# Optimization experiments

Hardware: AMD Instinct MI355X
Metric: run time of the kernel (lower is better)

Reference implementation:

```python
import jax, jax.numpy as jnp
import numpy as np

IDENT_SIZE = 100000
E = 1024      # embedding_dim == lstm input size
H = 2048      # hidden_dim
R = 1024      # remainder_dim
RULES = 50000 # rules_size


def setup_inputs() -> dict:
    key = jax.random.key(0)
    ks = jax.random.split(key, 12)
    def w(k, shape, scale=0.02):
        return jax.random.normal(k, shape, dtype=jnp.float32) * scale
    return {
        "ident": jax.random.randint(ks[0], (1,), 0, IDENT_SIZE),
        "remainder": jax.random.normal(ks[1], (1, 1, R), dtype=jnp.float32),
        "h0": jax.random.normal(ks[2], (1, 1, H), dtype=jnp.float32),
        "c0": jax.random.normal(ks[3], (1, 1, H), dtype=jnp.float32),
        "emb": w(ks[4], (IDENT_SIZE, E)),
        "W_rin": w(ks[5], (R, E)),   # linear_remainder_in, stored [in, out]
        "b_rin": jnp.zeros((E,), jnp.float32),
        "W_ih": w(ks[6], (4 * H, E)),  # torch LSTM weight_ih_l0, gate order i,f,g,o
        "W_hh": w(ks[7], (4 * H, H)),  # torch LSTM weight_hh_l0
        "b_ih": jnp.zeros((4 * H,), jnp.float32),
        "b_hh": jnp.zeros((4 * H,), jnp.float32),
        "W_ro": w(ks[8], (H, R)),      # linear_remainder_out
        "b_ro": jnp.zeros((R,), jnp.float32),
        "W_out": w(ks[9], (H, RULES)),  # linear_out
        "b_out": jnp.zeros((RULES,), jnp.float32),
    }


def reference(ident, remainder, h0, c0, emb, W_rin, b_rin, W_ih, W_hh,
              b_ih, b_hh, W_ro, b_ro, W_out, b_out):
    # embeds = embedding(ident).view((1,-1))  -> [1, E]
    embeds = emb[ident].reshape(1, -1)
    # inputs = embeds + relu(linear_remainder_in(remainder)) -> broadcast [1,1,E]
    x = embeds + jax.nn.relu(remainder @ W_rin + b_rin)  # [1,1,E]
    # single-step LSTM (seq=1, batch=1), torch gate order i, f, g, o
    gates = x @ W_ih.T + b_ih + h0 @ W_hh.T + b_hh  # [1,1,4H]
    i, f, g, o = jnp.split(gates, 4, axis=-1)
    c = jax.nn.sigmoid(f) * c0 + jax.nn.sigmoid(i) * jnp.tanh(g)
    h = jax.nn.sigmoid(o) * jnp.tanh(c)  # lstm_out == h for seq=1
    remainder_out = jax.nn.relu(h @ W_ro + b_ro)             # [1,1,R]
    out = jax.nn.log_softmax(jax.nn.relu(h @ W_out + b_out), axis=2)  # [1,1,RULES]
    return (out, (h, c), remainder_out)
```

## Files before the change

kernel.cpp:

```cpp
#include <hip/hip_runtime.h>
#include <math.h>

#define E_DIM 1024
#define H_DIM 2048
#define R_DIM 1024
#define RULES 50000

#define OUT_H  50000
#define OUT_C  52048
#define OUT_RO 54096

#define WS_XP    0
#define WS_X     8192
#define WS_H     9216
#define WS_PL    11264
#define WS_LOG   411264
#define WS_BSUM  461264
#define WS_PRO   461320

__device__ __forceinline__ float sigf(float x) { return 1.f / (1.f + expf(-x)); }

__global__ __launch_bounds__(256) void k_x_partial(const float* __restrict__ rem,
    const float* __restrict__ W_rin, float* __restrict__ xp)
{
    __shared__ float rs[128];
    int ec = blockIdx.x, rc = blockIdx.y;
    if (threadIdx.x < 128) rs[threadIdx.x] = rem[rc * 128 + threadIdx.x];
    __syncthreads();
    int e = ec * 256 + threadIdx.x;
    const float* base = W_rin + (size_t)rc * 128 * E_DIM + e;
    float acc = 0.f;
#pragma unroll 8
    for (int rr = 0; rr < 128; ++rr)
        acc = fmaf(rs[rr], base[(size_t)rr * E_DIM], acc);
    xp[rc * E_DIM + e] = acc;
}

__global__ __launch_bounds__(256) void k_x_final(const float* __restrict__ xp,
    const float* __restrict__ b_rin, const float* __restrict__ emb,
    const int* __restrict__ ident, float* __restrict__ x)
{
    int e = blockIdx.x * 256 + threadIdx.x;
    float s = 0.f;
#pragma unroll
    for (int rc = 0; rc < 8; ++rc) s += xp[rc * E_DIM + e];
    long long row = (long long)ident[0] * E_DIM;
    x[e] = emb[row + e] + fmaxf(s + b_rin[e], 0.f);
}

__global__ __launch_bounds__(256) void k_lstm(const float* __restrict__ x,
    const float* __restrict__ h0, const float* __restrict__ c0,
    const float* __restrict__ W_ih, const float* __restrict__ W_hh,
    const float* __restrict__ b_ih, const float* __restrict__ b_hh,
    float* __restrict__ d_out, float* __restrict__ ws_h)
{
    int k = blockIdx.x;
    int w = threadIdx.x >> 6, lane = threadIdx.x & 63;
    int j = w * H_DIM + k;
    const float4* Wi = (const float4*)(W_ih + (size_t)j * E_DIM);
    const float4* Wh = (const float4*)(W_hh + (size_t)j * H_DIM);
    const float4* x4 = (const float4*)x;
    const float4* h4 = (const float4*)h0;
    float acc = 0.f;
#pragma unroll
    for (int s = 0; s < 4; ++s) {
        int idx = s * 64 + lane;
        float4 wv = Wi[idx], xv = x4[idx];
        acc += wv.x * xv.x + wv.y * xv.y + wv.z * xv.z + wv.w * xv.w;
    }
#pragma unroll
    for (int s = 0; s < 8; ++s) {
        int idx = s * 64 + lane;
        float4 wv = Wh[idx], hv = h4[idx];
        acc += wv.x * hv.x + wv.y * hv.y + wv.z * hv.z + wv.w * hv.w;
    }
#pragma unroll
    for (int off = 32; off > 0; off >>= 1) acc += __shfl_xor(acc, off);
    __shared__ float gl[4];
    if (lane == 0) gl[w] = acc + b_ih[j] + b_hh[j];
    __syncthreads();
    if (threadIdx.x == 0) {
        float gi = gl[0], gf = gl[1], gg = gl[2], go = gl[3];
        float c = sigf(gf) * c0[k] + sigf(gi) * tanhf(gg);
        float h = sigf(go) * tanhf(c);
        d_out[OUT_H + k] = h;
        d_out[OUT_C + k] = c;
        ws_h[k] = h;
    }
}

__global__ __launch_bounds__(256) void k_logits_partial(const float* __restrict__ h,
    const float* __restrict__ W_out, float* __restrict__ pl)
{
    __shared__ float hs[256];
    int hc = blockIdx.y;
    hs[threadIdx.x] = h[hc * 256 + threadIdx.x];
    __syncthreads();
    int j0 = blockIdx.x * 1024 + threadIdx.x * 4;
    if (j0 >= RULES) return;
    float4 acc = {0.f, 0.f, 0.f, 0.f};
    const float* base = W_out + (size_t)hc * 256 * RULES + j0;
#pragma unroll 8
    for (int hh = 0; hh < 256; ++hh) {
        float hv = hs[hh];
        float4 wv = *(const float4*)(base + (size_t)hh * RULES);
        acc.x = fmaf(hv, wv.x, acc.x);
        acc.y = fmaf(hv, wv.y, acc.y);
        acc.z = fmaf(hv, wv.z, acc.z);
        acc.w = fmaf(hv, wv.w, acc.w);
    }
    *(float4*)(pl + (size_t)hc * RULES + j0) = acc;
}

__global__ __launch_bounds__(256) void k_ro_partial(const float* __restrict__ h,
    const float* __restrict__ W_ro, float* __restrict__ pro)
{
    __shared__ float hs[128];
    int hc = blockIdx.x;
    if (threadIdx.x < 128) hs[threadIdx.x] = h[hc * 128 + threadIdx.x];
    __syncthreads();
    int j0 = threadIdx.x * 4;
    float4 acc = {0.f, 0.f, 0.f, 0.f};
    const float* base = W_ro + (size_t)hc * 128 * R_DIM + j0;
#pragma unroll 8
    for (int hh = 0; hh < 128; ++hh) {
        float hv = hs[hh];
        float4 wv = *(const float4*)(base + (size_t)hh * R_DIM);
        acc.x = fmaf(hv, wv.x, acc.x);
        acc.y = fmaf(hv, wv.y, acc.y);
        acc.z = fmaf(hv, wv.z, acc.z);
        acc.w = fmaf(hv, wv.w, acc.w);
    }
    *(float4*)(pro + hc * R_DIM + j0) = acc;
}

__global__ __launch_bounds__(256) void k_logit_final(const float* __restrict__ pl,
    const float* __restrict__ b_out, float* __restrict__ logits,
    float* __restrict__ bsum)
{
    int j0 = blockIdx.x * 1024 + threadIdx.x * 4;
    float se = 0.f;
    if (j0 < RULES) {
        float4 s = {0.f, 0.f, 0.f, 0.f};
#pragma unroll
        for (int hc = 0; hc < 8; ++hc) {
            float4 p = *(const float4*)(pl + (size_t)hc * RULES + j0);
            s.x += p.x; s.y += p.y; s.z += p.z; s.w += p.w;
        }
        float4 b = *(const float4*)(b_out + j0);
        float4 l;
        l.x = fmaxf(s.x + b.x, 0.f);
        l.y = fmaxf(s.y + b.y, 0.f);
        l.z = fmaxf(s.z + b.z, 0.f);
        l.w = fmaxf(s.w + b.w, 0.f);
        *(float4*)(logits + j0) = l;
        se = expf(l.x) + expf(l.y) + expf(l.z) + expf(l.w);
    }
    __shared__ float red[256];
    red[threadIdx.x] = se;
    __syncthreads();
    for (int off = 128; off > 0; off >>= 1) {
        if (threadIdx.x < off) red[threadIdx.x] += red[threadIdx.x + off];
        __syncthreads();
    }
    if (threadIdx.x == 0) bsum[blockIdx.x] = red[0];
}

__global__ __launch_bounds__(256) void k_ro_final(const float* __restrict__ pro,
    const float* __restrict__ b_ro, float* __restrict__ out_ro)
{
    int j0 = threadIdx.x * 4;
    float4 s = {0.f, 0.f, 0.f, 0.f};
#pragma unroll
    for (int hc = 0; hc < 16; ++hc) {
        float4 p = *(const float4*)(pro + hc * R_DIM + j0);
        s.x += p.x; s.y += p.y; s.z += p.z; s.w += p.w;
    }
    float4 b = *(const float4*)(b_ro + j0);
    float4 o;
    o.x = fmaxf(s.x + b.x, 0.f);
    o.y = fmaxf(s.y + b.y, 0.f);
    o.z = fmaxf(s.z + b.z, 0.f);
    o.w = fmaxf(s.w + b.w, 0.f);
    *(float4*)(out_ro + j0) = o;
}

__global__ __launch_bounds__(256) void k_out(const float* __restrict__ logits,
    const float* __restrict__ bsum, float* __restrict__ d_out)
{
    __shared__ float lse_s;
    if (threadIdx.x == 0) {
        float s = 0.f;
        for (int i = 0; i < 49; ++i) s += bsum[i];
        lse_s = logf(s);
    }
    __syncthreads();
    int j = blockIdx.x * 256 + threadIdx.x;
    if (j < RULES) d_out[j] = logits[j] - lse_s;
}

extern "C" void kernel_launch(void* const* d_in, const int* in_sizes, int n_in,
                              void* d_out, int out_size, void* d_ws, size_t ws_size,
                              hipStream_t stream)
{
    const int*   ident = (const int*)  d_in[0];
    const float* rem   = (const float*)d_in[1];
    const float* h0    = (const float*)d_in[2];
    const float* c0    = (const float*)d_in[3];
    const float* emb   = (const float*)d_in[4];
    const float* W_rin = (const float*)d_in[5];
    const float* b_rin = (const float*)d_in[6];
    const float* W_ih  = (const float*)d_in[7];
    const float* W_hh  = (const float*)d_in[8];
    const float* b_ih  = (const float*)d_in[9];
    const float* b_hh  = (const float*)d_in[10];
    const float* W_ro  = (const float*)d_in[11];
    const float* b_ro  = (const float*)d_in[12];
    const float* W_out = (const float*)d_in[13];
    const float* b_out = (const float*)d_in[14];
    float* out = (float*)d_out;
    float* ws  = (float*)d_ws;

    k_x_partial<<<dim3(4, 8), 256, 0, stream>>>(rem, W_rin, ws + WS_XP);
    k_x_final<<<4, 256, 0, stream>>>(ws + WS_XP, b_rin, emb, ident, ws + WS_X);
    k_lstm<<<2048, 256, 0, stream>>>(ws + WS_X, h0, c0, W_ih, W_hh, b_ih, b_hh,
                                     out, ws + WS_H);
    k_logits_partial<<<dim3(49, 8), 256, 0, stream>>>(ws + WS_H, W_out, ws + WS_PL);
    k_ro_partial<<<16, 256, 0, stream>>>(ws + WS_H, W_ro, ws + WS_PRO);
    k_logit_final<<<49, 256, 0, stream>>>(ws + WS_PL, b_out, ws + WS_LOG, ws + WS_BSUM);
    k_ro_final<<<1, 256, 0, stream>>>(ws + WS_PRO, b_ro, out + OUT_RO);
    k_out<<<196, 256, 0, stream>>>(ws + WS_LOG, ws + WS_BSUM, out);
}
```

Before: 128.7 us.

## Fuse x-final into LSTM, merge logits/remainder kernels, split hidden dim 16-way

Folds the input-vector finalisation into each LSTM block, which rebuilds x in shared memory and so drops one launch. The logits and remainder-out partial GEMVs are merged into one launch, as are their reduce kernels. The logits split over the hidden dimension goes from 8 to 16 chunks, doubling block count for better bandwidth use. In exchange, every LSTM block redundantly reads the 8 x-partials and the embedding row, and the partial-sum buffer and its reduction double in size.

```diff
diff --git a/kernel.cpp b/kernel.cpp
--- a/kernel.cpp
+++ b/kernel.cpp
@@ -11,12 +11,11 @@
 #define OUT_RO 54096
 
 #define WS_XP    0
-#define WS_X     8192
-#define WS_H     9216
-#define WS_PL    11264
-#define WS_LOG   411264
-#define WS_BSUM  461264
-#define WS_PRO   461320
+#define WS_H     8192
+#define WS_PL    10240
+#define WS_LOG   810240
+#define WS_BSUM  860240
+#define WS_PRO   860292
 
 __device__ __forceinline__ float sigf(float x) { return 1.f / (1.f + expf(-x)); }
 
@@ -36,30 +35,31 @@
     xp[rc * E_DIM + e] = acc;
 }
 
-__global__ __launch_bounds__(256) void k_x_final(const float* __restrict__ xp,
+__global__ __launch_bounds__(256) void k_lstm(const float* __restrict__ xp,
     const float* __restrict__ b_rin, const float* __restrict__ emb,
-    const int* __restrict__ ident, float* __restrict__ x)
-{
-    int e = blockIdx.x * 256 + threadIdx.x;
-    float s = 0.f;
-#pragma unroll
-    for (int rc = 0; rc < 8; ++rc) s += xp[rc * E_DIM + e];
-    long long row = (long long)ident[0] * E_DIM;
-    x[e] = emb[row + e] + fmaxf(s + b_rin[e], 0.f);
-}
-
-__global__ __launch_bounds__(256) void k_lstm(const float* __restrict__ x,
+    const int* __restrict__ ident,
     const float* __restrict__ h0, const float* __restrict__ c0,
     const float* __restrict__ W_ih, const float* __restrict__ W_hh,
     const float* __restrict__ b_ih, const float* __restrict__ b_hh,
     float* __restrict__ d_out, float* __restrict__ ws_h)
 {
+    __shared__ float xs[E_DIM];
+    long long row = (long long)ident[0] * E_DIM;
+#pragma unroll
+    for (int e = threadIdx.x; e < E_DIM; e += 256) {
+        float s = 0.f;
+#pragma unroll
+        for (int rc = 0; rc < 8; ++rc) s += xp[rc * E_DIM + e];
+        xs[e] = emb[row + e] + fmaxf(s + b_rin[e], 0.f);
+    }
+    __syncthreads();
+
     int k = blockIdx.x;
     int w = threadIdx.x >> 6, lane = threadIdx.x & 63;
     int j = w * H_DIM + k;
     const float4* Wi = (const float4*)(W_ih + (size_t)j * E_DIM);
     const float4* Wh = (const float4*)(W_hh + (size_t)j * H_DIM);
-    const float4* x4 = (const float4*)x;
+    const float4* x4 = (const float4*)xs;
     const float4* h4 = (const float4*)h0;
     float acc = 0.f;
 #pragma unroll
@@ -89,100 +89,94 @@
     }
 }
 
-__global__ __launch_bounds__(256) void k_logits_partial(const float* __restrict__ h,
-    const float* __restrict__ W_out, float* __restrict__ pl)
-{
-    __shared__ float hs[256];
+__global__ __launch_bounds__(256) void k_big_partial(const float* __restrict__ h,
+    const float* __restrict__ W_out, const float* __restrict__ W_ro,
+    float* __restrict__ pl, float* __restrict__ pro)
+{
+    __shared__ float hs[128];
     int hc = blockIdx.y;
-    hs[threadIdx.x] = h[hc * 256 + threadIdx.x];
-    __syncthreads();
-    int j0 = blockIdx.x * 1024 + threadIdx.x * 4;
-    if (j0 >= RULES) return;
-    float4 acc = {0.f, 0.f, 0.f, 0.f};
-    const float* base = W_out + (size_t)hc * 256 * RULES + j0;
+    if (threadIdx.x < 128) hs[threadIdx.x] = h[hc * 128 + threadIdx.x];
+    __syncthreads();
+    if (blockIdx.x < 49) {
+        int j0 = blockIdx.x * 1024 + threadIdx.x * 4;
+        if (j0 >= RULES) return;
+        float4 acc = {0.f, 0.f, 0.f, 0.f};
+        const float* base = W_out + (size_t)hc * 128 * RULES + j0;
 #pragma unroll 8
-    for (int hh = 0; hh < 256; ++hh) {
-        float hv = hs[hh];
-        float4 wv = *(const float4*)(base + (size_t)hh * RULES);
-        acc.x = fmaf(hv, wv.x, acc.x);
-        acc.y = fmaf(hv, wv.y, acc.y);
-        acc.z = fmaf(hv, wv.z, acc.z);
-        acc.w = fmaf(hv, wv.w, acc.w);
-    }
-    *(float4*)(pl + (size_t)hc * RULES + j0) = acc;
-}
-
-__global__ __launch_bounds__(256) void k_ro_partial(const float* __restrict__ h,
-    const float* __restrict__ W_ro, float* __restrict__ pro)
-{
-    __shared__ float hs[128];
-    int hc = blockIdx.x;
-    if (threadIdx.x < 128) hs[threadIdx.x] = h[hc * 128 + threadIdx.x];
-    __syncthreads();
-    int j0 = threadIdx.x * 4;
-    float4 acc = {0.f, 0.f, 0.f, 0.f};
-    const float* base = W_ro + (size_t)hc * 128 * R_DIM + j0;
+        for (int hh = 0; hh < 128; ++hh) {
+            float hv = hs[hh];
+            float4 wv = *(const float4*)(base + (size_t)hh * RULES);
+            acc.x = fmaf(hv, wv.x, acc.x);
+            acc.y = fmaf(hv, wv.y, acc.y);
+            acc.z = fmaf(hv, wv.z, acc.z);
+            acc.w = fmaf(hv, wv.w, acc.w);
+        }
+        *(float4*)(pl + (size_t)hc * RULES + j0) = acc;
+    } else {
+        int j0 = threadIdx.x * 4;
+        float4 acc = {0.f, 0.f, 0.f, 0.f};
+        const float* base = W_ro + (size_t)hc * 128 * R_DIM + j0;
 #pragma unroll 8
-    for (int hh = 0; hh < 128; ++hh) {
-        float hv = hs[hh];
-        float4 wv = *(const float4*)(base + (size_t)hh * R_DIM);
-        acc.x = fmaf(hv, wv.x, acc.x);
-        acc.y = fmaf(hv, wv.y, acc.y);
-        acc.z = fmaf(hv, wv.z, acc.z);
-        acc.w = fmaf(hv, wv.w, acc.w);
-    }
-    *(float4*)(pro + hc * R_DIM + j0) = acc;
-}
-
-__global__ __launch_bounds__(256) void k_logit_final(const float* __restrict__ pl,
-    const float* __restrict__ b_out, float* __restrict__ logits,
-    float* __restrict__ bsum)
-{
-    int j0 = blockIdx.x * 1024 + threadIdx.x * 4;
-    float se = 0.f;
-    if (j0 < RULES) {
+        for (int hh = 0; hh < 128; ++hh) {
+            float hv = hs[hh];
+            float4 wv = *(const float4*)(base + (size_t)hh * R_DIM);
+            acc.x = fmaf(hv, wv.x, acc.x);
+            acc.y = fmaf(hv, wv.y, acc.y);
+            acc.z = fmaf(hv, wv.z, acc.z);
+            acc.w = fmaf(hv, wv.w, acc.w);
+        }
+        *(float4*)(pro + hc * R_DIM + j0) = acc;
+    }
+}
+
+__global__ __launch_bounds__(256) void k_final(const float* __restrict__ pl,
+    const float* __restrict__ b_out, const float* __restrict__ pro,
+    const float* __restrict__ b_ro, float* __restrict__ logits,
+    float* __restrict__ bsum, float* __restrict__ out_ro)
+{
+    if (blockIdx.x < 49) {
+        int j0 = blockIdx.x * 1024 + threadIdx.x * 4;
+        float se = 0.f;
+        if (j0 < RULES) {
+            float4 s = {0.f, 0.f, 0.f, 0.f};
+#pragma unroll
+            for (int hc = 0; hc < 16; ++hc) {
+                float4 p = *(const float4*)(pl + (size_t)hc * RULES + j0);
+                s.x += p.x; s.y += p.y; s.z += p.z; s.w += p.w;
+            }
+            float4 b = *(const float4*)(b_out + j0);
+            float4 l;
+            l.x = fmaxf(s.x + b.x, 0.f);
+            l.y = fmaxf(s.y + b.y, 0.f);
+            l.z = fmaxf(s.z + b.z, 0.f);
+            l.w = fmaxf(s.w + b.w, 0.f);
+            *(float4*)(logits + j0) = l;
+            se = expf(l.x) + expf(l.y) + expf(l.z) + expf(l.w);
+        }
+        __shared__ float red[256];
+        red[threadIdx.x] = se;
+        __syncthreads();
+        for (int off = 128; off > 0; off >>= 1) {
+            if (threadIdx.x < off) red[threadIdx.x] += red[threadIdx.x + off];
+            __syncthreads();
+        }
+        if (threadIdx.x == 0) bsum[blockIdx.x] = red[0];
+    } else {
+        int j0 = threadIdx.x * 4;
         float4 s = {0.f, 0.f, 0.f, 0.f};
 #pragma unroll
-        for (int hc = 0; hc < 8; ++hc) {
-            float4 p = *(const float4*)(pl + (size_t)hc * RULES + j0);
+        for (int hc = 0; hc < 16; ++hc) {
+            float4 p = *(const float4*)(pro + hc * R_DIM + j0);
             s.x += p.x; s.y += p.y; s.z += p.z; s.w += p.w;
         }
-        float4 b = *(const float4*)(b_out + j0);
-        float4 l;
-        l.x = fmaxf(s.x + b.x, 0.f);
-        l.y = fmaxf(s.y + b.y, 0.f);
-        l.z = fmaxf(s.z + b.z, 0.f);
-        l.w = fmaxf(s.w + b.w, 0.f);
-        *(float4*)(logits + j0) = l;
-        se = expf(l.x) + expf(l.y) + expf(l.z) + expf(l.w);
-    }
-    __shared__ float red[256];
-    red[threadIdx.x] = se;
-    __syncthreads();
-    for (int off = 128; off > 0; off >>= 1) {
-        if (threadIdx.x < off) red[threadIdx.x] += red[threadIdx.x + off];
-        __syncthreads();
-    }
-    if (threadIdx.x == 0) bsum[blockIdx.x] = red[0];
-}
-
-__global__ __launch_bounds__(256) void k_ro_final(const float* __restrict__ pro,
-    const float* __restrict__ b_ro, float* __restrict__ out_ro)
-{
-    int j0 = threadIdx.x * 4;
-    float4 s = {0.f, 0.f, 0.f, 0.f};
-#pragma unroll
-    for (int hc = 0; hc < 16; ++hc) {
-        float4 p = *(const float4*)(pro + hc * R_DIM + j0);
-        s.x += p.x; s.y += p.y; s.z += p.z; s.w += p.w;
-    }
-    float4 b = *(const float4*)(b_ro + j0);
-    float4 o;
-    o.x = fmaxf(s.x + b.x, 0.f);
-    o.y = fmaxf(s.y + b.y, 0.f);
-    o.z = fmaxf(s.z + b.z, 0.f);
-    o.w = fmaxf(s.w + b.w, 0.f);
-    *(float4*)(out_ro + j0) = o;
+        float4 b = *(const float4*)(b_ro + j0);
+        float4 o;
+        o.x = fmaxf(s.x + b.x, 0.f);
+        o.y = fmaxf(s.y + b.y, 0.f);
+        o.z = fmaxf(s.z + b.z, 0.f);
+        o.w = fmaxf(s.w + b.w, 0.f);
+        *(float4*)(out_ro + j0) = o;
+    }
 }
 
 __global__ __launch_bounds__(256) void k_out(const float* __restrict__ logits,
@@ -222,12 +216,12 @@
     float* ws  = (float*)d_ws;
 
     k_x_partial<<<dim3(4, 8), 256, 0, stream>>>(rem, W_rin, ws + WS_XP);
-    k_x_final<<<4, 256, 0, stream>>>(ws + WS_XP, b_rin, emb, ident, ws + WS_X);
-    k_lstm<<<2048, 256, 0, stream>>>(ws + WS_X, h0, c0, W_ih, W_hh, b_ih, b_hh,
+    k_lstm<<<2048, 256, 0, stream>>>(ws + WS_XP, b_rin, emb, ident,
+                                     h0, c0, W_ih, W_hh, b_ih, b_hh,
                                      out, ws + WS_H);
-    k_logits_partial<<<dim3(49, 8), 256, 0, stream>>>(ws + WS_H, W_out, ws + WS_PL);
-    k_ro_partial<<<16, 256, 0, stream>>>(ws + WS_H, W_ro, ws + WS_PRO);
-    k_logit_final<<<49, 256, 0, stream>>>(ws + WS_PL, b_out, ws + WS_LOG, ws + WS_BSUM);
-    k_ro_final<<<1, 256, 0, stream>>>(ws + WS_PRO, b_ro, out + OUT_RO);
+    k_big_partial<<<dim3(50, 16), 256, 0, stream>>>(ws + WS_H, W_out, W_ro,
+                                                    ws + WS_PL, ws + WS_PRO);
+    k_final<<<50, 256, 0, stream>>>(ws + WS_PL, b_out, ws + WS_PRO, b_ro,
+                                    ws + WS_LOG, ws + WS_BSUM, out + OUT_RO);
     k_out<<<196, 256, 0, stream>>>(ws + WS_LOG, ws + WS_BSUM, out);
 }
```

Result: faster. 123.1 us (-4.3%).
